# Kernel tuning notes

Hardware: AMD Instinct MI355X
Metric: run time of the kernel (lower is better)

The kernel has to match this reference:

```python
import jax, jax.numpy as jnp
import numpy as np

GROUP = 128          # GPTQ quantization group size
H = 2048             # hidden_size
I = 1408             # moe_intermediate_size
T = 16384            # routed tokens


def _pack_rows(v):
    # v: [in, out] int4 values -> [in//8, out] int32 (8 nibbles per int32 along input dim)
    v = v.reshape(v.shape[0] // 8, 8, v.shape[1]).astype(jnp.int32)
    sh = (4 * jnp.arange(8, dtype=jnp.int32))[None, :, None]
    return (v << sh).sum(axis=1).astype(jnp.int32)


def _pack_cols(v):
    # v: [groups, out] int4 values -> [groups, out//8] int32
    v = v.reshape(v.shape[0], v.shape[1] // 8, 8).astype(jnp.int32)
    sh = (4 * jnp.arange(8, dtype=jnp.int32))[None, None, :]
    return (v << sh).sum(axis=-1).astype(jnp.int32)


def _unpack_rows(qw):
    # [in//8, out] int32 -> [in, out] int4 values
    sh = 4 * jnp.arange(8, dtype=jnp.int32)
    v = (qw[:, None, :] >> sh[None, :, None]) & 0xF
    return v.reshape(qw.shape[0] * 8, qw.shape[1])


def _unpack_cols(qz):
    # [groups, out//8] int32 -> [groups, out] int4 values
    sh = 4 * jnp.arange(8, dtype=jnp.int32)
    v = (qz[:, :, None] >> sh[None, None, :]) & 0xF
    return v.reshape(qz.shape[0], qz.shape[1] * 8)


def _dequant(qw, qz, sc):
    # GPTQ dequant: W[k, n] = (q[k, n] - (zero[g(k), n] + 1)) * scale[g(k), n]
    w = _unpack_rows(qw).astype(sc.dtype)                      # [in, out]
    z = (_unpack_cols(qz) + 1).astype(sc.dtype)                # [groups, out]
    scale = jnp.repeat(sc, GROUP, axis=0)                      # [in, out]
    zero = jnp.repeat(z, GROUP, axis=0)                        # [in, out]
    return (w - zero) * scale


def setup_inputs() -> dict:
    key = jax.random.key(0)
    ks = jax.random.split(key, 10)
    x = jax.random.normal(ks[0], (T, H), dtype=jnp.float32)

    def make_quant(kq, kz, ksc, n_in, n_out):
        q = jax.random.randint(kq, (n_in, n_out), 0, 16, dtype=jnp.int32)
        z = jax.random.randint(kz, (n_in // GROUP, n_out), 0, 15, dtype=jnp.int32)
        sc = jax.random.uniform(ksc, (n_in // GROUP, n_out), dtype=jnp.float32,
                                minval=1e-3, maxval=2e-2)
        return _pack_rows(q), _pack_cols(z), sc

    qw_g, qz_g, sc_g = make_quant(ks[1], ks[2], ks[3], H, I)
    qw_u, qz_u, sc_u = make_quant(ks[4], ks[5], ks[6], H, I)
    qw_d, qz_d, sc_d = make_quant(ks[7], ks[8], ks[9], I, H)
    return {"x": x,
            "qw_gate": qw_g, "qz_gate": qz_g, "sc_gate": sc_g,
            "qw_up": qw_u, "qz_up": qz_u, "sc_up": sc_u,
            "qw_down": qw_d, "qz_down": qz_d, "sc_down": sc_d}


def reference(x, qw_gate, qz_gate, sc_gate, qw_up, qz_up, sc_up,
              qw_down, qz_down, sc_down):
    Wg = _dequant(qw_gate, qz_gate, sc_gate)   # [H, I]
    Wu = _dequant(qw_up, qz_up, sc_up)         # [H, I]
    Wd = _dequant(qw_down, qz_down, sc_down)   # [I, H]
    # fused_gate_up: silu(x @ Wg) * (x @ Wu)
    h = jax.nn.silu(x @ Wg) * (x @ Wu)         # [T, I]
    return h @ Wd                              # [T, H]
```

## Files before the change

kernel.cpp:

```cpp
#include <hip/hip_runtime.h>

#define T_DIM 16384
#define H_DIM 2048
#define I_DIM 1408
#define NB_DIM (2 * I_DIM)

typedef _Float16 half8 __attribute__((ext_vector_type(8)));
typedef float floatx4 __attribute__((ext_vector_type(4)));

__device__ __forceinline__ void async_cp16(const _Float16* gp, _Float16* lp) {
    __builtin_amdgcn_global_load_lds(
        (const __attribute__((address_space(1))) unsigned int*)gp,
        (__attribute__((address_space(3))) unsigned int*)lp,
        16, 0, 0);
}

__global__ void cvt_fp16_kernel(const float* __restrict__ x, _Float16* __restrict__ xh) {
    int i = (blockIdx.x * 256 + threadIdx.x) * 8;
    const float4* p = (const float4*)(x + i);
    float4 a = p[0];
    float4 b = p[1];
    half8 o = { (_Float16)a.x, (_Float16)a.y, (_Float16)a.z, (_Float16)a.w,
                (_Float16)b.x, (_Float16)b.y, (_Float16)b.z, (_Float16)b.w };
    *(half8*)(xh + i) = o;
}

__global__ void dequant_kernel(const int* __restrict__ qw, const int* __restrict__ qz,
                               const float* __restrict__ sc, _Float16* __restrict__ Wt,
                               int K, int N, int interleave, int off) {
    __shared__ half8 tile[256];
    int t = threadIdx.x;
    int nl = t & 63, kl = t >> 6;
    int n  = blockIdx.x * 64 + nl;
    int kp = blockIdx.y * 4 + kl;
    int q = qw[kp * N + n];
    int g = kp >> 4;
    float scale = sc[g * N + n];
    int zq = (qz[g * (N >> 3) + (n >> 3)] >> (4 * (n & 7))) & 0xF;
    float zf = (float)(zq + 1);
    half8 o;
#pragma unroll
    for (int j = 0; j < 8; ++j)
        o[j] = (_Float16)(((float)((q >> (4 * j)) & 0xF) - zf) * scale);
    tile[nl * 4 + kl] = o;
    __syncthreads();
    int nl2 = t >> 2, kl2 = t & 3;
    int n2 = blockIdx.x * 64 + nl2;
    int np = interleave ? (((n2 >> 5) << 6) + (n2 & 31) + off) : n2;
    *(half8*)(Wt + (size_t)np * K + (size_t)(blockIdx.y * 4 + kl2) * 8) = tile[nl2 * 4 + kl2];
}


__launch_bounds__(256, 4)
__global__ void gemm_gateup(const _Float16* __restrict__ A,
                            const _Float16* __restrict__ B,
                            _Float16* __restrict__ h) {
    __shared__ _Float16 As[128 * 64];
    __shared__ _Float16 Bs[128 * 64];
    const int t = threadIdx.x;
    const int wave = t >> 6, lane = t & 63;

    const int NPAN = NB_DIM / 128;
    const int per_super = 64 * NPAN;
    int id = blockIdx.x;
    int sup = id / per_super;
    int rem = id - sup * per_super;
    const int m0 = (sup * 64 + (rem & 63)) * 128;
    const int n_p = rem >> 6;
    const int n0 = n_p * 128;
    const int wm = wave >> 1, wn = wave & 1;

    const int srow = wave * 8 + (lane >> 3);
    const int schunk = (lane & 7) ^ (lane >> 3);
    const _Float16* ag = A + (size_t)(m0 + srow) * H_DIM + schunk * 8;
    const _Float16* bg = B + (size_t)(n0 + srow) * H_DIM + schunk * 8;
    _Float16* lA = As + wave * 512;
    _Float16* lB = Bs + wave * 512;

    const int q4 = lane >> 4, l15 = lane & 15;
    int aoff[4], boff[4];
#pragma unroll
    for (int i = 0; i < 4; ++i) {
        int rA = wm * 64 + i * 16 + l15;
        aoff[i] = rA * 64 + ((q4 ^ (rA & 7)) * 8);
        int rB = wn * 64 + i * 16 + l15;
        boff[i] = rB * 64 + ((q4 ^ (rB & 7)) * 8);
    }

    floatx4 zero = {0.f, 0.f, 0.f, 0.f};
    floatx4 acc[4][4];
#pragma unroll
    for (int mi = 0; mi < 4; ++mi)
#pragma unroll
        for (int ni = 0; ni < 4; ++ni) acc[mi][ni] = zero;

    for (int kt = 0; kt < H_DIM; kt += 64) {
        __syncthreads();
#pragma unroll
        for (int i = 0; i < 4; ++i) {
            async_cp16(ag + kt + (size_t)i * 32 * H_DIM, lA + i * 2048);
            async_cp16(bg + kt + (size_t)i * 32 * H_DIM, lB + i * 2048);
        }
        __syncthreads();
#pragma unroll
        for (int kk = 0; kk < 2; ++kk) {
            half8 af[4], bf[4];
#pragma unroll
            for (int i = 0; i < 4; ++i) af[i] = *(const half8*)(As + (aoff[i] ^ (kk * 32)));
#pragma unroll
            for (int i = 0; i < 4; ++i) bf[i] = *(const half8*)(Bs + (boff[i] ^ (kk * 32)));
#pragma unroll
            for (int mi = 0; mi < 4; ++mi)
#pragma unroll
                for (int ni = 0; ni < 4; ++ni)
                    acc[mi][ni] = __builtin_amdgcn_mfma_f32_16x16x32_f16(af[mi], bf[ni], acc[mi][ni], 0, 0, 0);
        }
    }

    const int rq = q4 * 4;
#pragma unroll
    for (int mi = 0; mi < 4; ++mi)
#pragma unroll
        for (int nc = 0; nc < 2; ++nc)
#pragma unroll
            for (int r = 0; r < 4; ++r) {
                int row = m0 + wm * 64 + mi * 16 + rq + r;
                int col = n_p * 64 + wn * 32 + nc * 16 + l15;
                float g = acc[mi][nc][r];
                float u = acc[mi][nc + 2][r];
                float s = (g / (1.0f + __expf(-g))) * u;
                h[(size_t)row * I_DIM + col] = (_Float16)s;
            }
}

__launch_bounds__(256, 4)
__global__ void gemm_down(const _Float16* __restrict__ A,
                          const _Float16* __restrict__ B,
                          float* __restrict__ out) {
    __shared__ _Float16 As[128 * 64];
    __shared__ _Float16 Bs[128 * 64];
    const int t = threadIdx.x;
    const int wave = t >> 6, lane = t & 63;

    const int NPAN = H_DIM / 128;
    const int per_super = 64 * NPAN;
    int id = blockIdx.x;
    int sup = id / per_super;
    int rem = id - sup * per_super;
    const int m0 = (sup * 64 + (rem & 63)) * 128;
    const int n0 = (rem >> 6) * 128;
    const int wm = wave >> 1, wn = wave & 1;

    const int srow = wave * 8 + (lane >> 3);
    const int schunk = (lane & 7) ^ (lane >> 3);
    const _Float16* ag = A + (size_t)(m0 + srow) * I_DIM + schunk * 8;
    const _Float16* bg = B + (size_t)(n0 + srow) * I_DIM + schunk * 8;
    _Float16* lA = As + wave * 512;
    _Float16* lB = Bs + wave * 512;

    const int q4 = lane >> 4, l15 = lane & 15;
    int aoff[4], boff[4];
#pragma unroll
    for (int i = 0; i < 4; ++i) {
        int rA = wm * 64 + i * 16 + l15;
        aoff[i] = rA * 64 + ((q4 ^ (rA & 7)) * 8);
        int rB = wn * 64 + i * 16 + l15;
        boff[i] = rB * 64 + ((q4 ^ (rB & 7)) * 8);
    }

    floatx4 zero = {0.f, 0.f, 0.f, 0.f};
    floatx4 acc[4][4];
#pragma unroll
    for (int mi = 0; mi < 4; ++mi)
#pragma unroll
        for (int ni = 0; ni < 4; ++ni) acc[mi][ni] = zero;

    for (int kt = 0; kt < I_DIM; kt += 64) {
        __syncthreads();
#pragma unroll
        for (int i = 0; i < 4; ++i) {
            async_cp16(ag + kt + (size_t)i * 32 * I_DIM, lA + i * 2048);
            async_cp16(bg + kt + (size_t)i * 32 * I_DIM, lB + i * 2048);
        }
        __syncthreads();
#pragma unroll
        for (int kk = 0; kk < 2; ++kk) {
            half8 af[4], bf[4];
#pragma unroll
            for (int i = 0; i < 4; ++i) af[i] = *(const half8*)(As + (aoff[i] ^ (kk * 32)));
#pragma unroll
            for (int i = 0; i < 4; ++i) bf[i] = *(const half8*)(Bs + (boff[i] ^ (kk * 32)));
#pragma unroll
            for (int mi = 0; mi < 4; ++mi)
#pragma unroll
                for (int ni = 0; ni < 4; ++ni)
                    acc[mi][ni] = __builtin_amdgcn_mfma_f32_16x16x32_f16(af[mi], bf[ni], acc[mi][ni], 0, 0, 0);
        }
    }

    const int rq = q4 * 4;
#pragma unroll
    for (int mi = 0; mi < 4; ++mi)
#pragma unroll
        for (int ni = 0; ni < 4; ++ni)
#pragma unroll
            for (int r = 0; r < 4; ++r) {
                int row = m0 + wm * 64 + mi * 16 + rq + r;
                int col = n0 + wn * 64 + ni * 16 + l15;
                out[(size_t)row * H_DIM + col] = acc[mi][ni][r];
            }
}

extern "C" void kernel_launch(void* const* d_in, const int* in_sizes, int n_in,
                              void* d_out, int out_size, void* d_ws, size_t ws_size,
                              hipStream_t stream) {
    const float* x    = (const float*)d_in[0];
    const int* qw_g   = (const int*)d_in[1];
    const int* qz_g   = (const int*)d_in[2];
    const float* sc_g = (const float*)d_in[3];
    const int* qw_u   = (const int*)d_in[4];
    const int* qz_u   = (const int*)d_in[5];
    const float* sc_u = (const float*)d_in[6];
    const int* qw_d   = (const int*)d_in[7];
    const int* qz_d   = (const int*)d_in[8];
    const float* sc_d = (const float*)d_in[9];
    float* out = (float*)d_out;

    char* ws = (char*)d_ws;
    _Float16* xh  = (_Float16*)ws;  ws += (size_t)T_DIM * H_DIM * sizeof(_Float16);
    _Float16* hh  = (_Float16*)ws;  ws += (size_t)T_DIM * I_DIM * sizeof(_Float16);
    _Float16* Bgu = (_Float16*)ws;  ws += (size_t)NB_DIM * H_DIM * sizeof(_Float16);
    _Float16* Wd  = (_Float16*)ws;  ws += (size_t)I_DIM * H_DIM * sizeof(_Float16);

    cvt_fp16_kernel<<<(T_DIM * H_DIM) / 2048, 256, 0, stream>>>(x, xh);
    dequant_kernel<<<dim3(I_DIM / 64, H_DIM / 32), 256, 0, stream>>>(qw_g, qz_g, sc_g, Bgu, H_DIM, I_DIM, 1, 0);
    dequant_kernel<<<dim3(I_DIM / 64, H_DIM / 32), 256, 0, stream>>>(qw_u, qz_u, sc_u, Bgu, H_DIM, I_DIM, 1, 32);
    dequant_kernel<<<dim3(H_DIM / 64, I_DIM / 32), 256, 0, stream>>>(qw_d, qz_d, sc_d, Wd, I_DIM, H_DIM, 0, 0);
    gemm_gateup<<<(T_DIM / 128) * (NB_DIM / 128), 256, 0, stream>>>(xh, Bgu, hh);
    gemm_down<<<(T_DIM / 128) * (H_DIM / 128), 256, 0, stream>>>(hh, Wd, out);
}
```

Before: 516.7 us.

## Replace GEMMs with 256x256 double-buffered 8-wave phased pipeline kernel

Both GEMMs now share one templated kernel. It computes 256x256 output tiles with 512 threads and double-buffered LDS, and splits each K-tile into four phases. In each phase the next tile's async global-to-LDS loads are issued while MFMAs run, with explicit vmcnt waits, barriers and setprio. The larger tiles cut global reloads of A and B and hide load latency behind compute. In exchange the kernel uses 128 KB of LDS, needs more registers and fewer blocks fit per CU, and it drops the supertile block-ordering swizzle.

New measurement: 520.7 us. Within noise of the previous version (+0.8%).

```diff
diff --git a/kernel.cpp b/kernel.cpp
--- a/kernel.cpp
+++ b/kernel.cpp
@@ -51,164 +51,141 @@
 }
 
 
-__launch_bounds__(256, 4)
-__global__ void gemm_gateup(const _Float16* __restrict__ A,
-                            const _Float16* __restrict__ B,
-                            _Float16* __restrict__ h) {
-    __shared__ _Float16 As[128 * 64];
-    __shared__ _Float16 Bs[128 * 64];
+#define STAGE_A(p, h, kt) do {                                                        \
+    async_cp16(ag + (size_t)((h) * 128) * KDIM + (size_t)(kt) * 64,                   \
+               &As[p][(h) * 8192 + ldst]);                                            \
+    async_cp16(ag + (size_t)((h) * 128 + 64) * KDIM + (size_t)(kt) * 64,              \
+               &As[p][(h) * 8192 + 4096 + ldst]);                                     \
+} while (0)
+
+#define STAGE_B(p, h, kt) do {                                                        \
+    async_cp16(bg + (size_t)((h) * 128) * KDIM + (size_t)(kt) * 64,                   \
+               &Bs[p][(h) * 8192 + ldst]);                                            \
+    async_cp16(bg + (size_t)((h) * 128 + 64) * KDIM + (size_t)(kt) * 64,              \
+               &Bs[p][(h) * 8192 + 4096 + ldst]);                                     \
+} while (0)
+
+#define PHASE(p, mh, nh, RA, RB, ...) do {                                            \
+    if (RA) {                                                                         \
+        _Pragma("unroll") for (int i_ = 0; i_ < 4; ++i_)                              \
+        _Pragma("unroll") for (int kk_ = 0; kk_ < 2; ++kk_)                           \
+            af[i_][kk_] = *(const half8*)&As[p][(mh) * 4096 + (aoff[i_] ^ (kk_ * 32))]; \
+    }                                                                                 \
+    if (RB) {                                                                         \
+        _Pragma("unroll") for (int j_ = 0; j_ < 2; ++j_)                              \
+        _Pragma("unroll") for (int kk_ = 0; kk_ < 2; ++kk_)                           \
+            bf[nh][j_][kk_] = *(const half8*)&Bs[p][(nh) * 2048 + (boff[j_] ^ (kk_ * 32))]; \
+    }                                                                                 \
+    __VA_ARGS__;                                                                      \
+    asm volatile("s_barrier" ::: "memory");                                           \
+    __builtin_amdgcn_s_setprio(1);                                                    \
+    _Pragma("unroll") for (int kk_ = 0; kk_ < 2; ++kk_)                               \
+    _Pragma("unroll") for (int i_ = 0; i_ < 4; ++i_)                                  \
+    _Pragma("unroll") for (int j_ = 0; j_ < 2; ++j_)                                  \
+        acc[(mh) * 4 + i_][(nh) * 2 + j_] = __builtin_amdgcn_mfma_f32_16x16x32_f16(   \
+            af[i_][kk_], bf[nh][j_][kk_], acc[(mh) * 4 + i_][(nh) * 2 + j_], 0, 0, 0);\
+    __builtin_amdgcn_s_setprio(0);                                                    \
+    asm volatile("s_barrier" ::: "memory");                                           \
+} while (0)
+
+#define TILE(p, kt) do {                                                              \
+    asm volatile("s_waitcnt vmcnt(4)" ::: "memory");                                  \
+    asm volatile("s_barrier" ::: "memory");                                           \
+    PHASE(p, 0, 0, 1, 1, if ((kt) + 1 < NT) STAGE_A(p ^ 1, 1, (kt) + 1));             \
+    PHASE(p, 0, 1, 0, 1, if ((kt) + 1 < NT) STAGE_B(p ^ 1, 1, (kt) + 1));             \
+    PHASE(p, 1, 0, 1, 0, if ((kt) + 2 < NT) STAGE_B(p, 0, (kt) + 2));                 \
+    PHASE(p, 1, 1, 0, 0, if ((kt) + 2 < NT) STAGE_A(p, 0, (kt) + 2));                 \
+} while (0)
+
+template<int KDIM, int EPI>
+__launch_bounds__(512, 2)
+__global__ void gemm256(const _Float16* __restrict__ A,
+                        const _Float16* __restrict__ B,
+                        void* __restrict__ Cout) {
+    constexpr int NT = KDIM / 64;
+    __shared__ __align__(16) _Float16 As[2][16384];
+    __shared__ __align__(16) _Float16 Bs[2][16384];
+
     const int t = threadIdx.x;
     const int wave = t >> 6, lane = t & 63;
-
-    const int NPAN = NB_DIM / 128;
-    const int per_super = 64 * NPAN;
-    int id = blockIdx.x;
-    int sup = id / per_super;
-    int rem = id - sup * per_super;
-    const int m0 = (sup * 64 + (rem & 63)) * 128;
-    const int n_p = rem >> 6;
-    const int n0 = n_p * 128;
-    const int wm = wave >> 1, wn = wave & 1;
+    const int id = blockIdx.x;
+    const int m0 = (id & 63) * 256;
+    const int n_p = id >> 6;
+    const int n0 = n_p * 256;
+    const int wm = wave >> 2, wn = wave & 3;
+    const int q4 = lane >> 4, l15 = lane & 15;
 
     const int srow = wave * 8 + (lane >> 3);
     const int schunk = (lane & 7) ^ (lane >> 3);
-    const _Float16* ag = A + (size_t)(m0 + srow) * H_DIM + schunk * 8;
-    const _Float16* bg = B + (size_t)(n0 + srow) * H_DIM + schunk * 8;
-    _Float16* lA = As + wave * 512;
-    _Float16* lB = Bs + wave * 512;
-
-    const int q4 = lane >> 4, l15 = lane & 15;
-    int aoff[4], boff[4];
+    const _Float16* ag = A + (size_t)(m0 + srow) * KDIM + schunk * 8;
+    const _Float16* bg = B + (size_t)(n0 + srow) * KDIM + schunk * 8;
+    const int ldst = wave * 512;
+
+    int aoff[4], boff[2];
 #pragma unroll
     for (int i = 0; i < 4; ++i) {
-        int rA = wm * 64 + i * 16 + l15;
+        int rA = wm * 128 + i * 16 + l15;
         aoff[i] = rA * 64 + ((q4 ^ (rA & 7)) * 8);
-        int rB = wn * 64 + i * 16 + l15;
-        boff[i] = rB * 64 + ((q4 ^ (rB & 7)) * 8);
+    }
+#pragma unroll
+    for (int j = 0; j < 2; ++j) {
+        int rB = wn * 64 + j * 16 + l15;
+        boff[j] = rB * 64 + ((q4 ^ (rB & 7)) * 8);
     }
 
     floatx4 zero = {0.f, 0.f, 0.f, 0.f};
-    floatx4 acc[4][4];
-#pragma unroll
-    for (int mi = 0; mi < 4; ++mi)
+    floatx4 acc[8][4];
+#pragma unroll
+    for (int mi = 0; mi < 8; ++mi)
 #pragma unroll
         for (int ni = 0; ni < 4; ++ni) acc[mi][ni] = zero;
 
-    for (int kt = 0; kt < H_DIM; kt += 64) {
-        __syncthreads();
-#pragma unroll
-        for (int i = 0; i < 4; ++i) {
-            async_cp16(ag + kt + (size_t)i * 32 * H_DIM, lA + i * 2048);
-            async_cp16(bg + kt + (size_t)i * 32 * H_DIM, lB + i * 2048);
-        }
-        __syncthreads();
-#pragma unroll
-        for (int kk = 0; kk < 2; ++kk) {
-            half8 af[4], bf[4];
-#pragma unroll
-            for (int i = 0; i < 4; ++i) af[i] = *(const half8*)(As + (aoff[i] ^ (kk * 32)));
-#pragma unroll
-            for (int i = 0; i < 4; ++i) bf[i] = *(const half8*)(Bs + (boff[i] ^ (kk * 32)));
-#pragma unroll
-            for (int mi = 0; mi < 4; ++mi)
-#pragma unroll
-                for (int ni = 0; ni < 4; ++ni)
-                    acc[mi][ni] = __builtin_amdgcn_mfma_f32_16x16x32_f16(af[mi], bf[ni], acc[mi][ni], 0, 0, 0);
-        }
-    }
-
-    const int rq = q4 * 4;
-#pragma unroll
-    for (int mi = 0; mi < 4; ++mi)
-#pragma unroll
-        for (int nc = 0; nc < 2; ++nc)
-#pragma unroll
-            for (int r = 0; r < 4; ++r) {
-                int row = m0 + wm * 64 + mi * 16 + rq + r;
-                int col = n_p * 64 + wn * 32 + nc * 16 + l15;
-                float g = acc[mi][nc][r];
-                float u = acc[mi][nc + 2][r];
-                float s = (g / (1.0f + __expf(-g))) * u;
-                h[(size_t)row * I_DIM + col] = (_Float16)s;
-            }
-}
-
-__launch_bounds__(256, 4)
-__global__ void gemm_down(const _Float16* __restrict__ A,
-                          const _Float16* __restrict__ B,
-                          float* __restrict__ out) {
-    __shared__ _Float16 As[128 * 64];
-    __shared__ _Float16 Bs[128 * 64];
-    const int t = threadIdx.x;
-    const int wave = t >> 6, lane = t & 63;
-
-    const int NPAN = H_DIM / 128;
-    const int per_super = 64 * NPAN;
-    int id = blockIdx.x;
-    int sup = id / per_super;
-    int rem = id - sup * per_super;
-    const int m0 = (sup * 64 + (rem & 63)) * 128;
-    const int n0 = (rem >> 6) * 128;
-    const int wm = wave >> 1, wn = wave & 1;
-
-    const int srow = wave * 8 + (lane >> 3);
-    const int schunk = (lane & 7) ^ (lane >> 3);
-    const _Float16* ag = A + (size_t)(m0 + srow) * I_DIM + schunk * 8;
-    const _Float16* bg = B + (size_t)(n0 + srow) * I_DIM + schunk * 8;
-    _Float16* lA = As + wave * 512;
-    _Float16* lB = Bs + wave * 512;
-
-    const int q4 = lane >> 4, l15 = lane & 15;
-    int aoff[4], boff[4];
-#pragma unroll
-    for (int i = 0; i < 4; ++i) {
-        int rA = wm * 64 + i * 16 + l15;
-        aoff[i] = rA * 64 + ((q4 ^ (rA & 7)) * 8);
-        int rB = wn * 64 + i * 16 + l15;
-        boff[i] = rB * 64 + ((q4 ^ (rB & 7)) * 8);
-    }
-
-    floatx4 zero = {0.f, 0.f, 0.f, 0.f};
-    floatx4 acc[4][4];
-#pragma unroll
-    for (int mi = 0; mi < 4; ++mi)
-#pragma unroll
-        for (int ni = 0; ni < 4; ++ni) acc[mi][ni] = zero;
-
-    for (int kt = 0; kt < I_DIM; kt += 64) {
-        __syncthreads();
-#pragma unroll
-        for (int i = 0; i < 4; ++i) {
-            async_cp16(ag + kt + (size_t)i * 32 * I_DIM, lA + i * 2048);
-            async_cp16(bg + kt + (size_t)i * 32 * I_DIM, lB + i * 2048);
-        }
-        __syncthreads();
-#pragma unroll
-        for (int kk = 0; kk < 2; ++kk) {
-            half8 af[4], bf[4];
-#pragma unroll
-            for (int i = 0; i < 4; ++i) af[i] = *(const half8*)(As + (aoff[i] ^ (kk * 32)));
-#pragma unroll
-            for (int i = 0; i < 4; ++i) bf[i] = *(const half8*)(Bs + (boff[i] ^ (kk * 32)));
-#pragma unroll
-            for (int mi = 0; mi < 4; ++mi)
-#pragma unroll
-                for (int ni = 0; ni < 4; ++ni)
-                    acc[mi][ni] = __builtin_amdgcn_mfma_f32_16x16x32_f16(af[mi], bf[ni], acc[mi][ni], 0, 0, 0);
-        }
-    }
-
-    const int rq = q4 * 4;
-#pragma unroll
-    for (int mi = 0; mi < 4; ++mi)
-#pragma unroll
-        for (int ni = 0; ni < 4; ++ni)
-#pragma unroll
-            for (int r = 0; r < 4; ++r) {
-                int row = m0 + wm * 64 + mi * 16 + rq + r;
-                int col = n0 + wn * 64 + ni * 16 + l15;
-                out[(size_t)row * H_DIM + col] = acc[mi][ni][r];
-            }
+    half8 af[4][2];
+    half8 bf[2][2][2];
+
+    STAGE_B(0, 0, 0);
+    STAGE_A(0, 0, 0);
+    STAGE_A(0, 1, 0);
+    STAGE_B(0, 1, 0);
+    STAGE_B(1, 0, 1);
+    STAGE_A(1, 0, 1);
+
+    for (int tt = 0; tt < NT; tt += 2) {
+        TILE(0, tt);
+        TILE(1, tt + 1);
+    }
+
+    if constexpr (EPI == 1) {
+        _Float16* hout = (_Float16*)Cout;
+        const int rbase = m0 + wm * 128 + q4 * 4;
+        const int colbase = (n_p * 4 + wn) * 32 + l15;
+#pragma unroll
+        for (int mi = 0; mi < 8; ++mi)
+#pragma unroll
+            for (int nc = 0; nc < 2; ++nc)
+#pragma unroll
+                for (int r = 0; r < 4; ++r) {
+                    int row = rbase + mi * 16 + r;
+                    int col = colbase + nc * 16;
+                    float g = acc[mi][nc][r];
+                    float u = acc[mi][nc + 2][r];
+                    float s = (g / (1.0f + __expf(-g))) * u;
+                    hout[(size_t)row * I_DIM + col] = (_Float16)s;
+                }
+    } else {
+        float* outp = (float*)Cout;
+        const int rbase = m0 + wm * 128 + q4 * 4;
+#pragma unroll
+        for (int mi = 0; mi < 8; ++mi)
+#pragma unroll
+            for (int ni = 0; ni < 4; ++ni)
+#pragma unroll
+                for (int r = 0; r < 4; ++r) {
+                    int row = rbase + mi * 16 + r;
+                    int col = n0 + wn * 64 + ni * 16 + l15;
+                    outp[(size_t)row * H_DIM + col] = acc[mi][ni][r];
+                }
+    }
 }
 
 extern "C" void kernel_launch(void* const* d_in, const int* in_sizes, int n_in,
@@ -236,6 +213,6 @@
     dequant_kernel<<<dim3(I_DIM / 64, H_DIM / 32), 256, 0, stream>>>(qw_g, qz_g, sc_g, Bgu, H_DIM, I_DIM, 1, 0);
     dequant_kernel<<<dim3(I_DIM / 64, H_DIM / 32), 256, 0, stream>>>(qw_u, qz_u, sc_u, Bgu, H_DIM, I_DIM, 1, 32);
     dequant_kernel<<<dim3(H_DIM / 64, I_DIM / 32), 256, 0, stream>>>(qw_d, qz_d, sc_d, Wd, I_DIM, H_DIM, 0, 0);
-    gemm_gateup<<<(T_DIM / 128) * (NB_DIM / 128), 256, 0, stream>>>(xh, Bgu, hh);
-    gemm_down<<<(T_DIM / 128) * (H_DIM / 128), 256, 0, stream>>>(hh, Wd, out);
-}
+    gemm256<H_DIM, 1><<<(T_DIM / 256) * (NB_DIM / 256), 512, 0, stream>>>(xh, Bgu, hh);
+    gemm256<I_DIM, 0><<<(T_DIM / 256) * (H_DIM / 256), 512, 0, stream>>>(hh, Wd, out);
+}
```
